# Performance work log

Measured on AMD Instinct MI355X. Metric: run time of the kernel, lower is better.

## Reference

```python
import jax, jax.numpy as jnp
import numpy as np

EPS = 1e-8  # smoothing_radius


def setup_inputs() -> dict:
    key = jax.random.key(0)
    ks = jax.random.split(key, 8)
    T, S, D = 2048, 1024, 3
    H, FIN, FOUT = 64, 7, 4
    return {
        "reference_length": jnp.ones((), jnp.float32),
        "source_points": jax.random.normal(ks[0], (S, D), jnp.float32),
        "target_points": jax.random.normal(ks[1], (T, D), jnp.float32),
        "source_strengths": jax.random.uniform(ks[2], (S,), jnp.float32),
        "source_area": jax.random.uniform(ks[3], (S,), jnp.float32),
        "source_normal": jax.random.normal(ks[4], (S, D), jnp.float32),
        "W1": jax.random.normal(ks[5], (FIN, H), jnp.float32) / np.sqrt(FIN),
        "b1": jnp.zeros((H,), jnp.float32),
        "W2": jax.random.normal(ks[6], (H, FOUT), jnp.float32) / np.sqrt(H),
        "b2": jnp.zeros((FOUT,), jnp.float32),
    }


def _legendre4(x):
    # First 4 Legendre polynomials P1..P4 (n_spherical_harmonics = 4)
    x2 = x * x
    p1 = x
    p2 = 0.5 * (3.0 * x2 - 1.0)
    p3 = 0.5 * (5.0 * x2 - 3.0) * x
    p4 = 0.125 * ((35.0 * x2 - 30.0) * x2 + 3.0)
    return jnp.stack([p1, p2, p3, p4], axis=-1)


def _kernel_forward(reference_length, source_points, target_points,
                    source_strengths, source_area, source_normal,
                    W1, b1, W2, b2):
    D = source_points.shape[-1]
    # Dimensionless relative positions: [T, S, D]
    r = (target_points[:, None, :] - source_points[None, :, :]) / reference_length
    r2 = jnp.sum(r * r, axis=-1) + EPS * EPS          # [T, S]
    n2 = jnp.sum(source_normal * source_normal, -1) + EPS * EPS  # [S]
    # Invariant features: source scalar, smoothed log-magnitudes, pair Legendre terms
    log_r = 0.5 * jnp.log(r2)                          # [T, S]
    log_n = 0.5 * jnp.log(n2)                          # [S]
    cos = jnp.einsum('tsd,sd->ts', r, source_normal) / jnp.sqrt(r2 * n2[None, :])
    feats = jnp.concatenate([
        jnp.broadcast_to(source_area[None, :, None], r2.shape + (1,)),
        log_r[..., None],
        jnp.broadcast_to(log_n[None, :, None], r2.shape + (1,)),
        _legendre4(cos),
    ], axis=-1)                                        # [T, S, 7]
    # MLP kernel network with tanh squashing (network_type='mlp')
    h = jax.nn.silu(feats @ W1 + b1)                   # [T, S, 64]
    out = jnp.tanh(h @ W2 + b2)                        # [T, S, 4]
    # Physical far-field decay: scalar ~ 1/r^{D-2}, vector ~ 1/r^{D-1}
    inv_r = jax.lax.rsqrt(r2)
    decay_s = inv_r ** (D - 2)
    decay_v = inv_r ** (D - 1)
    w = source_strengths[None, :]                      # [1, S]
    scalar = jnp.sum(w * decay_s * out[..., 0], axis=-1)  # [T]
    # Rotationally invariant vector reprojection: radial + 2 coeffs per non-radial vector
    r_hat = r * inv_r[..., None]
    n_hat = source_normal / jnp.sqrt(n2)[:, None]
    n_hat_b = jnp.broadcast_to(n_hat[None], r.shape)
    vec = (out[..., 1:2] * r_hat
           + out[..., 2:3] * n_hat_b
           + out[..., 3:4] * jnp.cross(r_hat, n_hat_b))  # [T, S, D]
    vector = jnp.einsum('ts,tsd->td', w * decay_v, vec)   # [T, D]
    return jnp.concatenate([scalar[:, None], vector], axis=-1)  # [T, 1+D]


def reference(reference_length, source_points, target_points, source_strengths,
              source_area, source_normal, W1, b1, W2, b2):
    return _kernel_forward(reference_length, source_points, target_points,
                           source_strengths, source_area, source_normal,
                           W1, b1, W2, b2)
```

## Files before the change

kernel.cpp:

```cpp
#include <hip/hip_runtime.h>

typedef __attribute__((ext_vector_type(4))) float f32x4;
typedef __attribute__((ext_vector_type(8))) short bf16x8;

#define EPS2 1e-16f
constexpr int PBLOCK = 256;
constexpr int BLOCK  = 256;
constexpr float LOG2E = 1.4426950408889634f;

__device__ __forceinline__ float rcpf_fast(float x){ return __builtin_amdgcn_rcpf(x); }
__device__ __forceinline__ float rsqf_fast(float x){ return __builtin_amdgcn_rsqf(x); }
__device__ __forceinline__ float exp2_fast(float x){ return __builtin_amdgcn_exp2f(x); }
__device__ __forceinline__ unsigned cvt_pk_bf16(float lo, float hi){
    unsigned d;
    asm("v_cvt_pk_bf16_f32 %0, %1, %2" : "=v"(d) : "v"(lo), "v"(hi));
    return d;
}
__device__ __forceinline__ bf16x8 as_frag(int4 v){
    union { int4 i; bf16x8 f; } u; u.i = v; return u.f;
}

__global__ void prep(const float* __restrict__ refLenP,
                     const float* __restrict__ srcP,
                     const float* __restrict__ srcN,
                     const float* __restrict__ wgtP,
                     const float* __restrict__ areaP,
                     const float* __restrict__ W1,
                     const float* __restrict__ b1,
                     const float* __restrict__ W2,
                     float* __restrict__ ws, int S)
{
    const int nSrcBlk = (S + PBLOCK - 1) / PBLOCK;
    const int bid = blockIdx.x;
    if (bid < nSrcBlk) {
        const int s = bid * PBLOCK + threadIdx.x;
        if (s < S) {
            const float invL = rcpf_fast(refLenP[0]);
            float px = srcP[s*3+0]*invL, py = srcP[s*3+1]*invL, pz = srcP[s*3+2]*invL;
            float nx = srcN[s*3+0], ny = srcN[s*3+1], nz = srcN[s*3+2];
            float n2 = fmaf(nx,nx, fmaf(ny,ny, nz*nz)) + EPS2;
            float inv_n = rsqf_fast(n2);
            float l2n = __log2f(n2);
            float4* sPA = (float4*)(ws + 384);
            float4* sNB = (float4*)(ws + 384 + 4*S);
            float*  sw  = ws + 384 + 8*S;
            sPA[s] = make_float4(px, py, pz, areaP[s]);
            sNB[s] = make_float4(nx*inv_n, ny*inv_n, nz*inv_n, l2n);
            sw[s]  = wgtP[s];
        }
    } else {
        const int t = threadIdx.x;
        unsigned* W1u = (unsigned*)ws;
        unsigned* W2u = (unsigned*)ws + 256;
        if (t < 64) {
            const int h = t;
            float v[8];
            v[0] = -LOG2E * W1[0*64 + h];
            v[1] = -0.5f  * W1[1*64 + h];
            v[2] = -0.5f  * W1[2*64 + h];
            v[3] = -LOG2E * W1[3*64 + h];
            v[4] = -LOG2E * W1[4*64 + h];
            v[5] = -LOG2E * W1[5*64 + h];
            v[6] = -LOG2E * W1[6*64 + h];
            v[7] = -LOG2E * b1[h];
            #pragma unroll
            for (int r = 0; r < 4; ++r)
                W1u[h*4 + r] = cvt_pk_bf16(v[2*r], v[2*r+1]);
        } else if (t < 192) {
            const int idx = t - 64;
            const int j = idx >> 5;
            const int u = idx & 31;
            const int kt = u >> 4;
            const int q  = (u >> 2) & 3;
            const int w  = u & 3;
            const int m = 32*kt + (w>>1)*16 + 4*q + (w&1)*2;
            float a = -2.0f * W2[ m      * 4 + j];
            float b = -2.0f * W2[(m + 1) * 4 + j];
            W2u[j*32 + u] = cvt_pk_bf16(a, b);
        }
    }
}

__global__ __launch_bounds__(BLOCK)
void bh_kernel(const float* __restrict__ refLenP,
               const float* __restrict__ tgtP,
               const float* __restrict__ b2,
               const float* __restrict__ ws,
               float* __restrict__ out,
               int S, int T)
{
    __shared__ float red[4][4];

    const int tid = threadIdx.x;
    const int wv  = tid >> 6;
    const int l   = tid & 63;
    const int col = l & 15;
    const int q   = l >> 4;
    const int t   = blockIdx.x;

    const unsigned* __restrict__ W1u = (const unsigned*)ws;
    const unsigned* __restrict__ W2u = (const unsigned*)ws + 256;
    const float4* __restrict__ sPA = (const float4*)(ws + 384);
    const float4* __restrict__ sNB = (const float4*)(ws + 384 + 4*S);
    const float*  __restrict__ sw  = ws + 384 + 8*S;

    int4 A1[4];
    #pragma unroll
    for (int mt = 0; mt < 4; ++mt) {
        int4 r = *(const int4*)&W1u[(mt*16 + col) * 4];
        A1[mt] = (q == 0) ? r : make_int4(0,0,0,0);
    }
    int4 A2[2];
    #pragma unroll
    for (int kt = 0; kt < 2; ++kt) {
        const int rowj = col;
        const int src = (rowj < 4) ? rowj : 0;
        int4 r = *(const int4*)&W2u[src*32 + kt*16 + q*4];
        A2[kt] = (rowj < 4) ? r : make_int4(0,0,0,0);
    }

    const float invL = rcpf_fast(refLenP[0]);
    const float tx = tgtP[t*3+0]*invL;
    const float ty = tgtP[t*3+1]*invL;
    const float tz = tgtP[t*3+2]*invL;
    const float s2 = 2.0f * LOG2E;
    const f32x4 b2init = { s2*b2[0], s2*b2[1], s2*b2[2], s2*b2[3] };
    const f32x4 zero4  = { 0.f, 0.f, 0.f, 0.f };

    float acc0 = 0.f, acc1 = 0.f, acc2 = 0.f, acc3 = 0.f;

    for (int it = 0; it < 4; ++it) {
        const int s  = wv*256 + it*64 + l;
        const int sc = (s < S) ? s : 0;
        const float4 pa = sPA[sc];
        const float4 nb = sNB[sc];
        const float wgt = (s < S) ? sw[sc] : 0.f;

        float rx = tx - pa.x, ry = ty - pa.y, rz = tz - pa.z;
        float r2 = fmaf(rx,rx, fmaf(ry,ry, fmaf(rz,rz, EPS2)));
        float ir = rsqf_fast(r2);
        float l2r = __log2f(r2);
        float cosv = fmaf(rx,nb.x, fmaf(ry,nb.y, rz*nb.z)) * ir;
        float c2 = cosv * cosv;
        float P2 = fmaf(c2, 1.5f, -0.5f);
        float P3 = (c2*2.5f - 1.5f) * cosv;
        float P4 = fmaf(fmaf(c2, 4.375f, -3.75f), c2, 0.375f);
        unsigned fp0 = cvt_pk_bf16(pa.w, l2r);
        unsigned fp1 = cvt_pk_bf16(nb.w, cosv);
        unsigned fp2 = cvt_pk_bf16(P2,   P3);
        unsigned fp3 = cvt_pk_bf16(P4,   1.0f);

        f32x4 ov = zero4;

        #pragma unroll
        for (int pb = 0; pb < 4; ++pb) {
            const int srcl = pb*16 + col;
            int4 b1i = make_int4((int)__shfl(fp0, srcl), (int)__shfl(fp1, srcl),
                                 (int)__shfl(fp2, srcl), (int)__shfl(fp3, srcl));
            bf16x8 B1 = as_frag(b1i);

            unsigned pk[4][2];
            #pragma unroll
            for (int mt = 0; mt < 4; ++mt) {
                f32x4 c1 = __builtin_amdgcn_mfma_f32_16x16x32_bf16(
                               as_frag(A1[mt]), B1, zero4, 0, 0, 0);
                float hv0, hv1, hv2, hv3;
                { float e = exp2_fast(c1[0]); hv0 = c1[0] * rcpf_fast(1.0f + e); }
                { float e = exp2_fast(c1[1]); hv1 = c1[1] * rcpf_fast(1.0f + e); }
                { float e = exp2_fast(c1[2]); hv2 = c1[2] * rcpf_fast(1.0f + e); }
                { float e = exp2_fast(c1[3]); hv3 = c1[3] * rcpf_fast(1.0f + e); }
                pk[mt][0] = cvt_pk_bf16(hv0, hv1);
                pk[mt][1] = cvt_pk_bf16(hv2, hv3);
            }

            int4 B2a = make_int4((int)pk[0][0], (int)pk[0][1], (int)pk[1][0], (int)pk[1][1]);
            int4 B2b = make_int4((int)pk[2][0], (int)pk[2][1], (int)pk[3][0], (int)pk[3][1]);
            f32x4 oacc = b2init;
            oacc = __builtin_amdgcn_mfma_f32_16x16x32_bf16(as_frag(A2[0]), as_frag(B2a), oacc, 0, 0, 0);
            oacc = __builtin_amdgcn_mfma_f32_16x16x32_bf16(as_frag(A2[1]), as_frag(B2b), oacc, 0, 0, 0);

            #pragma unroll
            for (int k = 0; k < 4; ++k) {
                float tmp = __shfl(oacc[k], col);
                ov[k] = (q == pb) ? tmp : ov[k];
            }
        }

        float tt[4];
        #pragma unroll
        for (int k = 0; k < 4; ++k) {
            float m = __builtin_amdgcn_fmed3f(ov[k], -126.f, 126.f);
            float E = exp2_fast(m);
            tt[k] = (E - 1.0f) * rcpf_fast(E + 1.0f);
        }
        float wsv = wgt * ir;
        float wvv = wsv * ir;
        acc0 = fmaf(wsv, tt[0], acc0);
        float rhx = rx*ir, rhy = ry*ir, rhz = rz*ir;
        float cxx = rhy*nb.z - rhz*nb.y;
        float cxy = rhz*nb.x - rhx*nb.z;
        float cxz = rhx*nb.y - rhy*nb.x;
        float vx = tt[1]*rhx + tt[2]*nb.x + tt[3]*cxx;
        float vy = tt[1]*rhy + tt[2]*nb.y + tt[3]*cxy;
        float vz = tt[1]*rhz + tt[2]*nb.z + tt[3]*cxz;
        acc1 = fmaf(wvv, vx, acc1);
        acc2 = fmaf(wvv, vy, acc2);
        acc3 = fmaf(wvv, vz, acc3);
    }

    #pragma unroll
    for (int off = 32; off > 0; off >>= 1) {
        acc0 += __shfl_down(acc0, off);
        acc1 += __shfl_down(acc1, off);
        acc2 += __shfl_down(acc2, off);
        acc3 += __shfl_down(acc3, off);
    }
    if ((tid & 63) == 0) {
        red[wv][0] = acc0; red[wv][1] = acc1;
        red[wv][2] = acc2; red[wv][3] = acc3;
    }
    __syncthreads();
    if (tid < 4) {
        float v = red[0][tid] + red[1][tid] + red[2][tid] + red[3][tid];
        out[t*4 + tid] = v;
    }
}

extern "C" void kernel_launch(void* const* d_in, const int* in_sizes, int n_in,
                              void* d_out, int out_size, void* d_ws, size_t ws_size,
                              hipStream_t stream) {
    const float* refLen = (const float*)d_in[0];
    const float* srcP   = (const float*)d_in[1];
    const float* tgtP   = (const float*)d_in[2];
    const float* w      = (const float*)d_in[3];
    const float* area   = (const float*)d_in[4];
    const float* srcN   = (const float*)d_in[5];
    const float* W1     = (const float*)d_in[6];
    const float* b1     = (const float*)d_in[7];
    const float* W2     = (const float*)d_in[8];
    const float* b2     = (const float*)d_in[9];
    float* out          = (float*)d_out;
    float* ws           = (float*)d_ws;

    const int S = in_sizes[3];
    const int T = in_sizes[2] / 3;
    const int nSrcBlk = (S + PBLOCK - 1) / PBLOCK;

    prep<<<nSrcBlk + 1, PBLOCK, 0, stream>>>(refLen, srcP, srcN, w, area, W1, b1, W2, ws, S);
    bh_kernel<<<T, BLOCK, 0, stream>>>(refLen, tgtP, b2, ws, out, S, T);
}
```

Baseline: 110.5 us.

## Split source range across four blocks per target with atomic accumulation

Each target's 1024 sources are now split across four blocks, one 256-source chunk each, so every wave handles a single 64-source iteration. Launching four times as many blocks is meant to raise occupancy and latency hiding. Partial sums are combined with atomicAdd into an output that the prep kernel now zeroes, and launch bounds request 6 blocks per SIMD. The cost is more atomic traffic, repeated setup of weight fragments per block, and a hardcoded chunk count that assumes S is at most 1024.

```diff
diff --git a/kernel.cpp b/kernel.cpp
--- a/kernel.cpp
+++ b/kernel.cpp
@@ -28,7 +28,8 @@
                      const float* __restrict__ W1,
                      const float* __restrict__ b1,
                      const float* __restrict__ W2,
-                     float* __restrict__ ws, int S)
+                     float* __restrict__ ws,
+                     float* __restrict__ outZ, int outN, int S)
 {
     const int nSrcBlk = (S + PBLOCK - 1) / PBLOCK;
     const int bid = blockIdx.x;
@@ -48,7 +49,7 @@
             sNB[s] = make_float4(nx*inv_n, ny*inv_n, nz*inv_n, l2n);
             sw[s]  = wgtP[s];
         }
-    } else {
+    } else if (bid == nSrcBlk) {
         const int t = threadIdx.x;
         unsigned* W1u = (unsigned*)ws;
         unsigned* W2u = (unsigned*)ws + 256;
@@ -78,10 +79,13 @@
             float b = -2.0f * W2[(m + 1) * 4 + j];
             W2u[j*32 + u] = cvt_pk_bf16(a, b);
         }
-    }
-}
-
-__global__ __launch_bounds__(BLOCK)
+    } else {
+        const int i = (bid - nSrcBlk - 1) * PBLOCK + threadIdx.x;
+        if (i < outN) outZ[i] = 0.0f;
+    }
+}
+
+__global__ __launch_bounds__(BLOCK, 6)
 void bh_kernel(const float* __restrict__ refLenP,
                const float* __restrict__ tgtP,
                const float* __restrict__ b2,
@@ -96,7 +100,9 @@
     const int l   = tid & 63;
     const int col = l & 15;
     const int q   = l >> 4;
-    const int t   = blockIdx.x;
+    const int bid = blockIdx.x;
+    const int t     = bid >> 2;
+    const int chunk = bid & 3;
 
     const unsigned* __restrict__ W1u = (const unsigned*)ws;
     const unsigned* __restrict__ W2u = (const unsigned*)ws + 256;
@@ -127,86 +133,82 @@
     const f32x4 b2init = { s2*b2[0], s2*b2[1], s2*b2[2], s2*b2[3] };
     const f32x4 zero4  = { 0.f, 0.f, 0.f, 0.f };
 
-    float acc0 = 0.f, acc1 = 0.f, acc2 = 0.f, acc3 = 0.f;
-
-    for (int it = 0; it < 4; ++it) {
-        const int s  = wv*256 + it*64 + l;
-        const int sc = (s < S) ? s : 0;
-        const float4 pa = sPA[sc];
-        const float4 nb = sNB[sc];
-        const float wgt = (s < S) ? sw[sc] : 0.f;
-
-        float rx = tx - pa.x, ry = ty - pa.y, rz = tz - pa.z;
-        float r2 = fmaf(rx,rx, fmaf(ry,ry, fmaf(rz,rz, EPS2)));
-        float ir = rsqf_fast(r2);
-        float l2r = __log2f(r2);
-        float cosv = fmaf(rx,nb.x, fmaf(ry,nb.y, rz*nb.z)) * ir;
-        float c2 = cosv * cosv;
-        float P2 = fmaf(c2, 1.5f, -0.5f);
-        float P3 = (c2*2.5f - 1.5f) * cosv;
-        float P4 = fmaf(fmaf(c2, 4.375f, -3.75f), c2, 0.375f);
-        unsigned fp0 = cvt_pk_bf16(pa.w, l2r);
-        unsigned fp1 = cvt_pk_bf16(nb.w, cosv);
-        unsigned fp2 = cvt_pk_bf16(P2,   P3);
-        unsigned fp3 = cvt_pk_bf16(P4,   1.0f);
-
-        f32x4 ov = zero4;
-
+    const int s  = chunk*256 + wv*64 + l;
+    const int sc = (s < S) ? s : 0;
+    const float4 pa = sPA[sc];
+    const float4 nb = sNB[sc];
+    const float wgt = (s < S) ? sw[sc] : 0.f;
+
+    float rx = tx - pa.x, ry = ty - pa.y, rz = tz - pa.z;
+    float r2 = fmaf(rx,rx, fmaf(ry,ry, fmaf(rz,rz, EPS2)));
+    float ir = rsqf_fast(r2);
+    float l2r = __log2f(r2);
+    float cosv = fmaf(rx,nb.x, fmaf(ry,nb.y, rz*nb.z)) * ir;
+    float c2 = cosv * cosv;
+    float P2 = fmaf(c2, 1.5f, -0.5f);
+    float P3 = (c2*2.5f - 1.5f) * cosv;
+    float P4 = fmaf(fmaf(c2, 4.375f, -3.75f), c2, 0.375f);
+    unsigned fp0 = cvt_pk_bf16(pa.w, l2r);
+    unsigned fp1 = cvt_pk_bf16(nb.w, cosv);
+    unsigned fp2 = cvt_pk_bf16(P2,   P3);
+    unsigned fp3 = cvt_pk_bf16(P4,   1.0f);
+
+    f32x4 ov = zero4;
+
+    #pragma unroll
+    for (int pb = 0; pb < 4; ++pb) {
+        const int srcl = pb*16 + col;
+        int4 b1i = make_int4((int)__shfl(fp0, srcl), (int)__shfl(fp1, srcl),
+                             (int)__shfl(fp2, srcl), (int)__shfl(fp3, srcl));
+        bf16x8 B1 = as_frag(b1i);
+
+        unsigned pk[4][2];
         #pragma unroll
-        for (int pb = 0; pb < 4; ++pb) {
-            const int srcl = pb*16 + col;
-            int4 b1i = make_int4((int)__shfl(fp0, srcl), (int)__shfl(fp1, srcl),
-                                 (int)__shfl(fp2, srcl), (int)__shfl(fp3, srcl));
-            bf16x8 B1 = as_frag(b1i);
-
-            unsigned pk[4][2];
-            #pragma unroll
-            for (int mt = 0; mt < 4; ++mt) {
-                f32x4 c1 = __builtin_amdgcn_mfma_f32_16x16x32_bf16(
-                               as_frag(A1[mt]), B1, zero4, 0, 0, 0);
-                float hv0, hv1, hv2, hv3;
-                { float e = exp2_fast(c1[0]); hv0 = c1[0] * rcpf_fast(1.0f + e); }
-                { float e = exp2_fast(c1[1]); hv1 = c1[1] * rcpf_fast(1.0f + e); }
-                { float e = exp2_fast(c1[2]); hv2 = c1[2] * rcpf_fast(1.0f + e); }
-                { float e = exp2_fast(c1[3]); hv3 = c1[3] * rcpf_fast(1.0f + e); }
-                pk[mt][0] = cvt_pk_bf16(hv0, hv1);
-                pk[mt][1] = cvt_pk_bf16(hv2, hv3);
-            }
-
-            int4 B2a = make_int4((int)pk[0][0], (int)pk[0][1], (int)pk[1][0], (int)pk[1][1]);
-            int4 B2b = make_int4((int)pk[2][0], (int)pk[2][1], (int)pk[3][0], (int)pk[3][1]);
-            f32x4 oacc = b2init;
-            oacc = __builtin_amdgcn_mfma_f32_16x16x32_bf16(as_frag(A2[0]), as_frag(B2a), oacc, 0, 0, 0);
-            oacc = __builtin_amdgcn_mfma_f32_16x16x32_bf16(as_frag(A2[1]), as_frag(B2b), oacc, 0, 0, 0);
-
-            #pragma unroll
-            for (int k = 0; k < 4; ++k) {
-                float tmp = __shfl(oacc[k], col);
-                ov[k] = (q == pb) ? tmp : ov[k];
-            }
-        }
-
-        float tt[4];
+        for (int mt = 0; mt < 4; ++mt) {
+            f32x4 c1 = __builtin_amdgcn_mfma_f32_16x16x32_bf16(
+                           as_frag(A1[mt]), B1, zero4, 0, 0, 0);
+            float hv0, hv1, hv2, hv3;
+            { float e = exp2_fast(c1[0]); hv0 = c1[0] * rcpf_fast(1.0f + e); }
+            { float e = exp2_fast(c1[1]); hv1 = c1[1] * rcpf_fast(1.0f + e); }
+            { float e = exp2_fast(c1[2]); hv2 = c1[2] * rcpf_fast(1.0f + e); }
+            { float e = exp2_fast(c1[3]); hv3 = c1[3] * rcpf_fast(1.0f + e); }
+            pk[mt][0] = cvt_pk_bf16(hv0, hv1);
+            pk[mt][1] = cvt_pk_bf16(hv2, hv3);
+        }
+
+        int4 B2a = make_int4((int)pk[0][0], (int)pk[0][1], (int)pk[1][0], (int)pk[1][1]);
+        int4 B2b = make_int4((int)pk[2][0], (int)pk[2][1], (int)pk[3][0], (int)pk[3][1]);
+        f32x4 oacc = b2init;
+        oacc = __builtin_amdgcn_mfma_f32_16x16x32_bf16(as_frag(A2[0]), as_frag(B2a), oacc, 0, 0, 0);
+        oacc = __builtin_amdgcn_mfma_f32_16x16x32_bf16(as_frag(A2[1]), as_frag(B2b), oacc, 0, 0, 0);
+
         #pragma unroll
         for (int k = 0; k < 4; ++k) {
-            float m = __builtin_amdgcn_fmed3f(ov[k], -126.f, 126.f);
-            float E = exp2_fast(m);
-            tt[k] = (E - 1.0f) * rcpf_fast(E + 1.0f);
-        }
-        float wsv = wgt * ir;
-        float wvv = wsv * ir;
-        acc0 = fmaf(wsv, tt[0], acc0);
-        float rhx = rx*ir, rhy = ry*ir, rhz = rz*ir;
-        float cxx = rhy*nb.z - rhz*nb.y;
-        float cxy = rhz*nb.x - rhx*nb.z;
-        float cxz = rhx*nb.y - rhy*nb.x;
-        float vx = tt[1]*rhx + tt[2]*nb.x + tt[3]*cxx;
-        float vy = tt[1]*rhy + tt[2]*nb.y + tt[3]*cxy;
-        float vz = tt[1]*rhz + tt[2]*nb.z + tt[3]*cxz;
-        acc1 = fmaf(wvv, vx, acc1);
-        acc2 = fmaf(wvv, vy, acc2);
-        acc3 = fmaf(wvv, vz, acc3);
-    }
+            float tmp = __shfl(oacc[k], col);
+            ov[k] = (q == pb) ? tmp : ov[k];
+        }
+    }
+
+    float tt[4];
+    #pragma unroll
+    for (int k = 0; k < 4; ++k) {
+        float m = __builtin_amdgcn_fmed3f(ov[k], -126.f, 126.f);
+        float E = exp2_fast(m);
+        tt[k] = (E - 1.0f) * rcpf_fast(E + 1.0f);
+    }
+    float wsv = wgt * ir;
+    float wvv = wsv * ir;
+    float acc0 = wsv * tt[0];
+    float rhx = rx*ir, rhy = ry*ir, rhz = rz*ir;
+    float cxx = rhy*nb.z - rhz*nb.y;
+    float cxy = rhz*nb.x - rhx*nb.z;
+    float cxz = rhx*nb.y - rhy*nb.x;
+    float vx = tt[1]*rhx + tt[2]*nb.x + tt[3]*cxx;
+    float vy = tt[1]*rhy + tt[2]*nb.y + tt[3]*cxy;
+    float vz = tt[1]*rhz + tt[2]*nb.z + tt[3]*cxz;
+    float acc1 = wvv * vx;
+    float acc2 = wvv * vy;
+    float acc3 = wvv * vz;
 
     #pragma unroll
     for (int off = 32; off > 0; off >>= 1) {
@@ -215,14 +217,14 @@
         acc2 += __shfl_down(acc2, off);
         acc3 += __shfl_down(acc3, off);
     }
-    if ((tid & 63) == 0) {
+    if (l == 0) {
         red[wv][0] = acc0; red[wv][1] = acc1;
         red[wv][2] = acc2; red[wv][3] = acc3;
     }
     __syncthreads();
     if (tid < 4) {
         float v = red[0][tid] + red[1][tid] + red[2][tid] + red[3][tid];
-        out[t*4 + tid] = v;
+        atomicAdd(&out[t*4 + tid], v);
     }
 }
 
@@ -245,7 +247,9 @@
     const int S = in_sizes[3];
     const int T = in_sizes[2] / 3;
     const int nSrcBlk = (S + PBLOCK - 1) / PBLOCK;
-
-    prep<<<nSrcBlk + 1, PBLOCK, 0, stream>>>(refLen, srcP, srcN, w, area, W1, b1, W2, ws, S);
-    bh_kernel<<<T, BLOCK, 0, stream>>>(refLen, tgtP, b2, ws, out, S, T);
-}
+    const int nZeroBlk = (out_size + PBLOCK - 1) / PBLOCK;
+
+    prep<<<nSrcBlk + 1 + nZeroBlk, PBLOCK, 0, stream>>>(
+        refLen, srcP, srcN, w, area, W1, b1, W2, ws, out, out_size, S);
+    bh_kernel<<<T * 4, BLOCK, 0, stream>>>(refLen, tgtP, b2, ws, out, S, T);
+}
```

Measured after the change: 107.7 us. 2.5% less time.
